# Kernel optimization log

Measured on AMD Instinct MI355X. Metric: run time of the kernel, lower is better.

The kernel has to match this reference:

```python
import jax, jax.numpy as jnp
import numpy as np

D = 512
N_WAY = 64
K_SHOT = 16
N_QUERY = 8192


def setup_inputs() -> dict:
    key = jax.random.key(0)
    k1, k2, k3, k4 = jax.random.split(key, 4)
    support = jax.random.normal(k1, (N_WAY * K_SHOT, D), dtype=jnp.float32)
    query = jax.random.normal(k2, (N_QUERY, D), dtype=jnp.float32)
    # nn.Linear(input_dim, input_dim) params (kaiming-uniform-ish scale)
    bound = 1.0 / np.sqrt(D)
    W = jax.random.uniform(k3, (D, D), minval=-bound, maxval=bound, dtype=jnp.float32)
    b = jax.random.uniform(k4, (D,), minval=-bound, maxval=bound, dtype=jnp.float32)
    return {"support": support, "query": query, "W": W, "b": b,
            "n_way": N_WAY, "k_shot": K_SHOT}


def reference(support, query, W, b, n_way, k_shot):
    # shared linear projection: x @ W^T + b (torch nn.Linear convention)
    support_emb = support @ W.T + b            # [n_way*k_shot, d]
    query_emb = query @ W.T + b                # [n_q, d]
    # class prototypes: mean over the k_shot axis
    prototypes = support_emb.reshape(n_way, k_shot, -1).mean(axis=1)  # [n_way, d]
    # pairwise squared euclidean distances (broadcast sub/square/sum,
    # same math as the torch euclidean_dist)
    diff = query_emb[:, None, :] - prototypes[None, :, :]  # [n_q, n_way, d]
    dists = jnp.sum(diff * diff, axis=-1)                  # [n_q, n_way]
    return dists
```

## Files before the change

kernel.cpp:

```cpp
#include <hip/hip_runtime.h>
#include <hip/hip_bf16.h>

#define D 512
#define NWAY 64
#define KSHOT 16
#define NQ 8192
#define BM 64

typedef __bf16 bf16_t;
typedef __bf16 bf16x8_t __attribute__((ext_vector_type(8)));
typedef __bf16 bf16x4_t __attribute__((ext_vector_type(4)));
typedef float  f32x4    __attribute__((ext_vector_type(4)));

typedef __attribute__((address_space(1))) const void gv_t;
typedef __attribute__((address_space(3))) void lv_t;
__device__ __forceinline__ void ld16(const void* g, void* l) {
    __builtin_amdgcn_global_load_lds((gv_t*)g, (lv_t*)l, 16, 0, 0);
}


__global__ __launch_bounds__(256) void k_prep(
    const float* __restrict__ sup, const float* __restrict__ W,
    const float* __restrict__ bias, bf16_t* __restrict__ Bsw,
    bf16_t* __restrict__ Psw)
{
    const int b = blockIdx.x, t = threadIdx.x;

    if (b < 256) {
        const int c = b >> 2, jq = b & 3;
        __shared__ __align__(16) float cm[D];
        {
            const int d = t * 2;
            float sx = 0.f, sy = 0.f;
#pragma unroll
            for (int j = 0; j < KSHOT; ++j) {
                float2 v = *(const float2*)(sup + (size_t)(c * KSHOT + j) * D + d);
                sx += v.x; sy += v.y;
            }
            cm[d] = sx * (1.0f / KSHOT); cm[d + 1] = sy * (1.0f / KSHOT);
        }
        __syncthreads();
        const int j = jq * 128 + (t >> 1);
        const int half = t & 1;
        const f32x4* wr = (const f32x4*)(W + (size_t)j * D + half * 256);
        const f32x4* cr = (const f32x4*)(cm + half * 256);
        float s = 0.f;
#pragma unroll 8
        for (int i = 0; i < 64; ++i) {
            f32x4 a = cr[i], wv = wr[i];
            s += a[0]*wv[0] + a[1]*wv[1] + a[2]*wv[2] + a[3]*wv[3];
        }
        s += __shfl_xor(s, 1);
        if (!half) {
            const float v = s + bias[j];
            const int sP = j >> 3;
            const int pos = (sP & ~7) | ((sP & 7) ^ (c & 7));
            Psw[c * 512 + pos * 8 + (j & 7)] = (bf16_t)v;
        }
        return;
    }

    {
        const int n = (b - 256) * 4 + (t >> 6);
        const int sl = t & 63;
        const f32x4* wp = (const f32x4*)(W + (size_t)n * D + sl * 8);
        f32x4 v0 = wp[0], v1 = wp[1];
        bf16x8_t hv = { (bf16_t)v0[0], (bf16_t)v0[1], (bf16_t)v0[2], (bf16_t)v0[3],
                        (bf16_t)v1[0], (bf16_t)v1[1], (bf16_t)v1[2], (bf16_t)v1[3] };
        const int ck = sl >> 3, s = sl & 7;
        *(bf16x8_t*)(Bsw + (size_t)ck * 32768 + n * 64 + ((s ^ (n & 7)) * 8)) = hv;
    }
}

__global__ __launch_bounds__(512, 2) void k_main(
    const float* __restrict__ query, const bf16_t* __restrict__ Bsw,
    const bf16_t* __restrict__ Psw, const float* __restrict__ bias,
    float* __restrict__ out)
{
    __shared__ __align__(16) bf16_t Bb[2][32768];
    __shared__ __align__(16) bf16_t Ab[2][4096];
    __shared__ float qln[4][BM];
    __shared__ float phs[NWAY];
    __shared__ float bs[512];

    const int t = threadIdx.x, bm = blockIdx.x;
    bs[t] = bias[t];

    const int l = t & 63, w = t >> 6;
    const int wm = w & 1, wn = w >> 1;
    const int r15 = l & 15, quad = l >> 4;

    const int xt0 = ((quad ^ (r15 & 7)) * 8);
    const int xt1 = (((4 + quad) ^ (r15 & 7)) * 8);
    const int aoff0 = (wm * 32 + r15) * 64;
    const int aoff1 = (wm * 32 + 16 + r15) * 64;
    const int boff = (wn * 128 + r15) * 64;

    const int am = t >> 3;
    const int as = t & 7;
    const int a_lds = am * 64 + ((as ^ (am & 7)) * 8);
    const float* aqp = query + (size_t)(bm * BM + am) * D + as * 8;

    bf16x8_t areg[8];
#pragma unroll
    for (int ck = 0; ck < 8; ++ck) {
        f32x4 v0 = *(const f32x4*)(aqp + ck * 64);
        f32x4 v1 = *(const f32x4*)(aqp + ck * 64 + 4);
        areg[ck] = (bf16x8_t){ (bf16_t)v0[0], (bf16_t)v0[1], (bf16_t)v0[2], (bf16_t)v0[3],
                               (bf16_t)v1[0], (bf16_t)v1[1], (bf16_t)v1[2], (bf16_t)v1[3] };
    }

    f32x4 acc[2][8];
#pragma unroll
    for (int rt = 0; rt < 2; ++rt)
#pragma unroll
        for (int i = 0; i < 8; ++i) acc[rt][i] = (f32x4){0.f, 0.f, 0.f, 0.f};

    {
#pragma unroll
        for (int i = 0; i < 8; ++i) {
            const int off = t * 8 + i * 4096;
            ld16(Bsw + off, &Bb[0][off]);
        }
        *(bf16x8_t*)(&Ab[0][a_lds]) = areg[0];
    }
    __syncthreads();

#pragma unroll
    for (int ck = 0; ck < 8; ++ck) {
        const int cur = ck & 1;
        if (ck < 7) {
            const int nxt = cur ^ 1;
            const size_t sb = (size_t)(ck + 1) * 32768;
#pragma unroll
            for (int i = 0; i < 8; ++i) {
                const int off = t * 8 + i * 4096;
                ld16(Bsw + sb + off, &Bb[nxt][off]);
            }
            *(bf16x8_t*)(&Ab[nxt][a_lds]) = areg[ck + 1];
        } else {
#pragma unroll
            for (int i = 0; i < 8; ++i) {
                const int off = t * 8 + i * 4096;
                ld16(Psw + off, &Bb[0][off]);
            }
        }

        bf16x8_t a00 = *(const bf16x8_t*)(&Ab[cur][aoff0 + xt0]);
        bf16x8_t a01 = *(const bf16x8_t*)(&Ab[cur][aoff0 + xt1]);
        bf16x8_t a10 = *(const bf16x8_t*)(&Ab[cur][aoff1 + xt0]);
        bf16x8_t a11 = *(const bf16x8_t*)(&Ab[cur][aoff1 + xt1]);
#pragma unroll
        for (int tt = 0; tt < 8; ++tt) {
            bf16x8_t b0 = *(const bf16x8_t*)(&Bb[cur][boff + tt * 1024 + xt0]);
            bf16x8_t b1 = *(const bf16x8_t*)(&Bb[cur][boff + tt * 1024 + xt1]);
            acc[0][tt] = __builtin_amdgcn_mfma_f32_16x16x32_bf16(a00, b0, acc[0][tt], 0, 0, 0);
            acc[0][tt] = __builtin_amdgcn_mfma_f32_16x16x32_bf16(a01, b1, acc[0][tt], 0, 0, 0);
            acc[1][tt] = __builtin_amdgcn_mfma_f32_16x16x32_bf16(a10, b0, acc[1][tt], 0, 0, 0);
            acc[1][tt] = __builtin_amdgcn_mfma_f32_16x16x32_bf16(a11, b1, acc[1][tt], 0, 0, 0);
        }

        if (ck < 7) __syncthreads();
    }
    __syncthreads();

    bf16_t* Ex = &Bb[1][0];
    float qp[2][4] = {{0.f,0.f,0.f,0.f},{0.f,0.f,0.f,0.f}};
#pragma unroll
    for (int tt = 0; tt < 8; ++tt) {
        const int k = wn * 128 + tt * 16 + r15;
        const int s = k >> 3, klo = k & 7;
        const float bv = bs[k];
#pragma unroll
        for (int rt = 0; rt < 2; ++rt)
#pragma unroll
        for (int reg = 0; reg < 4; ++reg) {
            const int row = wm * 32 + rt * 16 + quad * 4 + reg;
            const float v = acc[rt][tt][reg] + bv;
            qp[rt][reg] += v * v;
            const int pos = (s & ~7) | ((s & 7) ^ (row & 7));
            Ex[row * 512 + pos * 8 + klo] = (bf16_t)v;
        }
    }
#pragma unroll
    for (int rt = 0; rt < 2; ++rt)
#pragma unroll
    for (int reg = 0; reg < 4; ++reg) {
        float s = qp[rt][reg];
        s += __shfl_xor(s, 1); s += __shfl_xor(s, 2);
        s += __shfl_xor(s, 4); s += __shfl_xor(s, 8);
        if (r15 == 0) qln[wn][wm * 32 + rt * 16 + quad * 4 + reg] = s;
    }

    if (t < NWAY) {
        const bf16_t* pr = &Bb[0][t * 512];
        float s2 = 0.f;
#pragma unroll
        for (int i = 0; i < 64; ++i) {
            bf16x8_t v = *(const bf16x8_t*)(pr + i * 8);
#pragma unroll
            for (int e = 0; e < 8; ++e) { float f = (float)v[e]; s2 += f * f; }
        }
        phs[t] = s2;
    }
    __syncthreads();

    const int ert = w >> 1, ecg = w & 1;
    f32x4 cacc[2];
    cacc[0] = (f32x4){0.f, 0.f, 0.f, 0.f};
    cacc[1] = (f32x4){0.f, 0.f, 0.f, 0.f};
    const bf16_t* Pl = &Bb[0][0];
#pragma unroll
    for (int kk = 0; kk < 16; ++kk) {
        const int s = kk * 4 + quad;
        const int posA = (s & ~7) | ((s & 7) ^ (r15 & 7));
        bf16x8_t af = *(const bf16x8_t*)(Ex + (ert * 16 + r15) * 512 + posA * 8);
#pragma unroll
        for (int j = 0; j < 2; ++j) {
            bf16x8_t bf = *(const bf16x8_t*)(Pl + ((ecg * 2 + j) * 16 + r15) * 512 + posA * 8);
            cacc[j] = __builtin_amdgcn_mfma_f32_16x16x32_bf16(af, bf, cacc[j], 0, 0, 0);
        }
    }

#pragma unroll
    for (int reg = 0; reg < 4; ++reg) {
        const int row_local = ert * 16 + quad * 4 + reg;
        const float qt = qln[0][row_local] + qln[1][row_local] +
                         qln[2][row_local] + qln[3][row_local];
        const int rowg = bm * BM + row_local;
#pragma unroll
        for (int j = 0; j < 2; ++j) {
            const int c = (ecg * 2 + j) * 16 + r15;
            out[(size_t)rowg * NWAY + c] = qt + phs[c] - 2.0f * cacc[j][reg];
        }
    }
}

extern "C" void kernel_launch(void* const* d_in, const int* in_sizes, int n_in,
                              void* d_out, int out_size, void* d_ws, size_t ws_size,
                              hipStream_t stream)
{
    const float* support = (const float*)d_in[0];
    const float* query   = (const float*)d_in[1];
    const float* W       = (const float*)d_in[2];
    const float* bias    = (const float*)d_in[3];
    float* out = (float*)d_out;

    char* ws = (char*)d_ws;
    bf16_t* Bsw = (bf16_t*)ws;
    bf16_t* Psw = (bf16_t*)(ws + 524288);

    k_prep<<<384, 256, 0, stream>>>(support, W, bias, Bsw, Psw);
    k_main<<<128, 512, 0, stream>>>(query, Bsw, Psw, bias, out);
}
```

Baseline: 101.9 us.

## Split projection feature dimension across two blocks with atomic output accumulation

Each query tile is now handled by two blocks, each computing half of the projected features and partial norms and dot products, combined through atomicAdd into a zeroed output. This doubles the grid to fill more CUs and halves LDS per block. It adds a memset, atomic traffic, and duplicated query loading and conversion.

```diff
diff --git a/kernel.cpp b/kernel.cpp
--- a/kernel.cpp
+++ b/kernel.cpp
@@ -5,7 +5,6 @@
 #define NWAY 64
 #define KSHOT 16
 #define NQ 8192
-#define BM 64
 
 typedef __bf16 bf16_t;
 typedef __bf16 bf16x8_t __attribute__((ext_vector_type(8)));
@@ -77,14 +76,17 @@
     const bf16_t* __restrict__ Psw, const float* __restrict__ bias,
     float* __restrict__ out)
 {
-    __shared__ __align__(16) bf16_t Bb[2][32768];
+    __shared__ __align__(16) bf16_t Bb[2][16384];
     __shared__ __align__(16) bf16_t Ab[2][4096];
-    __shared__ float qln[4][BM];
+    __shared__ float qln[4][64];
     __shared__ float phs[NWAY];
-    __shared__ float bs[512];
-
-    const int t = threadIdx.x, bm = blockIdx.x;
-    bs[t] = bias[t];
+    __shared__ float bs[256];
+
+    const int t = threadIdx.x;
+    const int bm = blockIdx.x >> 1;
+    const int h  = blockIdx.x & 1;
+
+    if (t < 256) bs[t] = bias[h * 256 + t];
 
     const int l = t & 63, w = t >> 6;
     const int wm = w & 1, wn = w >> 1;
@@ -94,12 +96,12 @@
     const int xt1 = (((4 + quad) ^ (r15 & 7)) * 8);
     const int aoff0 = (wm * 32 + r15) * 64;
     const int aoff1 = (wm * 32 + 16 + r15) * 64;
-    const int boff = (wn * 128 + r15) * 64;
+    const int boff = (wn * 64 + r15) * 64;
 
     const int am = t >> 3;
     const int as = t & 7;
     const int a_lds = am * 64 + ((as ^ (am & 7)) * 8);
-    const float* aqp = query + (size_t)(bm * BM + am) * D + as * 8;
+    const float* aqp = query + (size_t)(bm * 64 + am) * D + as * 8;
 
     bf16x8_t areg[8];
 #pragma unroll
@@ -110,20 +112,19 @@
                                (bf16_t)v1[0], (bf16_t)v1[1], (bf16_t)v1[2], (bf16_t)v1[3] };
     }
 
-    f32x4 acc[2][8];
+    f32x4 acc[2][4];
 #pragma unroll
     for (int rt = 0; rt < 2; ++rt)
 #pragma unroll
-        for (int i = 0; i < 8; ++i) acc[rt][i] = (f32x4){0.f, 0.f, 0.f, 0.f};
-
-    {
-#pragma unroll
-        for (int i = 0; i < 8; ++i) {
-            const int off = t * 8 + i * 4096;
-            ld16(Bsw + off, &Bb[0][off]);
-        }
-        *(bf16x8_t*)(&Ab[0][a_lds]) = areg[0];
-    }
+        for (int i = 0; i < 4; ++i) acc[rt][i] = (f32x4){0.f, 0.f, 0.f, 0.f};
+
+    const int hbase = h * 16384;
+#pragma unroll
+    for (int i = 0; i < 4; ++i) {
+        const int off = t * 8 + i * 4096;
+        ld16(Bsw + hbase + off, &Bb[0][off]);
+    }
+    *(bf16x8_t*)(&Ab[0][a_lds]) = areg[0];
     __syncthreads();
 
 #pragma unroll
@@ -131,18 +132,19 @@
         const int cur = ck & 1;
         if (ck < 7) {
             const int nxt = cur ^ 1;
-            const size_t sb = (size_t)(ck + 1) * 32768;
-#pragma unroll
-            for (int i = 0; i < 8; ++i) {
+            const size_t sb = (size_t)(ck + 1) * 32768 + hbase;
+#pragma unroll
+            for (int i = 0; i < 4; ++i) {
                 const int off = t * 8 + i * 4096;
                 ld16(Bsw + sb + off, &Bb[nxt][off]);
             }
             *(bf16x8_t*)(&Ab[nxt][a_lds]) = areg[ck + 1];
         } else {
 #pragma unroll
-            for (int i = 0; i < 8; ++i) {
+            for (int i = 0; i < 4; ++i) {
                 const int off = t * 8 + i * 4096;
-                ld16(Psw + off, &Bb[0][off]);
+                const int c = off >> 8, j = off & 255;
+                ld16(Psw + c * 512 + h * 256 + j, &Bb[0][off]);
             }
         }
 
@@ -151,7 +153,7 @@
         bf16x8_t a10 = *(const bf16x8_t*)(&Ab[cur][aoff1 + xt0]);
         bf16x8_t a11 = *(const bf16x8_t*)(&Ab[cur][aoff1 + xt1]);
 #pragma unroll
-        for (int tt = 0; tt < 8; ++tt) {
+        for (int tt = 0; tt < 4; ++tt) {
             bf16x8_t b0 = *(const bf16x8_t*)(&Bb[cur][boff + tt * 1024 + xt0]);
             bf16x8_t b1 = *(const bf16x8_t*)(&Bb[cur][boff + tt * 1024 + xt1]);
             acc[0][tt] = __builtin_amdgcn_mfma_f32_16x16x32_bf16(a00, b0, acc[0][tt], 0, 0, 0);
@@ -167,8 +169,8 @@
     bf16_t* Ex = &Bb[1][0];
     float qp[2][4] = {{0.f,0.f,0.f,0.f},{0.f,0.f,0.f,0.f}};
 #pragma unroll
-    for (int tt = 0; tt < 8; ++tt) {
-        const int k = wn * 128 + tt * 16 + r15;
+    for (int tt = 0; tt < 4; ++tt) {
+        const int k = wn * 64 + tt * 16 + r15;
         const int s = k >> 3, klo = k & 7;
         const float bv = bs[k];
 #pragma unroll
@@ -179,7 +181,7 @@
             const float v = acc[rt][tt][reg] + bv;
             qp[rt][reg] += v * v;
             const int pos = (s & ~7) | ((s & 7) ^ (row & 7));
-            Ex[row * 512 + pos * 8 + klo] = (bf16_t)v;
+            Ex[row * 256 + pos * 8 + klo] = (bf16_t)v;
         }
     }
 #pragma unroll
@@ -193,10 +195,10 @@
     }
 
     if (t < NWAY) {
-        const bf16_t* pr = &Bb[0][t * 512];
+        const bf16_t* pr = &Bb[0][t * 256];
         float s2 = 0.f;
 #pragma unroll
-        for (int i = 0; i < 64; ++i) {
+        for (int i = 0; i < 32; ++i) {
             bf16x8_t v = *(const bf16x8_t*)(pr + i * 8);
 #pragma unroll
             for (int e = 0; e < 8; ++e) { float f = (float)v[e]; s2 += f * f; }
@@ -205,33 +207,34 @@
     }
     __syncthreads();
 
-    const int ert = w >> 1, ecg = w & 1;
+    const int rt2 = w >> 1, cg = w & 1;
     f32x4 cacc[2];
     cacc[0] = (f32x4){0.f, 0.f, 0.f, 0.f};
     cacc[1] = (f32x4){0.f, 0.f, 0.f, 0.f};
     const bf16_t* Pl = &Bb[0][0];
 #pragma unroll
-    for (int kk = 0; kk < 16; ++kk) {
+    for (int kk = 0; kk < 8; ++kk) {
         const int s = kk * 4 + quad;
         const int posA = (s & ~7) | ((s & 7) ^ (r15 & 7));
-        bf16x8_t af = *(const bf16x8_t*)(Ex + (ert * 16 + r15) * 512 + posA * 8);
+        bf16x8_t af = *(const bf16x8_t*)(Ex + (rt2 * 16 + r15) * 256 + posA * 8);
 #pragma unroll
         for (int j = 0; j < 2; ++j) {
-            bf16x8_t bf = *(const bf16x8_t*)(Pl + ((ecg * 2 + j) * 16 + r15) * 512 + posA * 8);
+            bf16x8_t bf = *(const bf16x8_t*)(Pl + ((cg * 2 + j) * 16 + r15) * 256 + posA * 8);
             cacc[j] = __builtin_amdgcn_mfma_f32_16x16x32_bf16(af, bf, cacc[j], 0, 0, 0);
         }
     }
 
 #pragma unroll
     for (int reg = 0; reg < 4; ++reg) {
-        const int row_local = ert * 16 + quad * 4 + reg;
+        const int row_local = rt2 * 16 + quad * 4 + reg;
         const float qt = qln[0][row_local] + qln[1][row_local] +
                          qln[2][row_local] + qln[3][row_local];
-        const int rowg = bm * BM + row_local;
+        const int rowg = bm * 64 + row_local;
 #pragma unroll
         for (int j = 0; j < 2; ++j) {
-            const int c = (ecg * 2 + j) * 16 + r15;
-            out[(size_t)rowg * NWAY + c] = qt + phs[c] - 2.0f * cacc[j][reg];
+            const int c = (cg * 2 + j) * 16 + r15;
+            atomicAdd(&out[(size_t)rowg * NWAY + c],
+                      qt + phs[c] - 2.0f * cacc[j][reg]);
         }
     }
 }
@@ -250,6 +253,7 @@
     bf16_t* Bsw = (bf16_t*)ws;
     bf16_t* Psw = (bf16_t*)(ws + 524288);
 
+    hipMemsetAsync(out, 0, (size_t)NQ * NWAY * sizeof(float), stream);
     k_prep<<<384, 256, 0, stream>>>(support, W, bias, Bsw, Psw);
-    k_main<<<128, 512, 0, stream>>>(query, Bsw, Psw, bias, out);
-}
+    k_main<<<256, 512, 0, stream>>>(query, Bsw, Psw, bias, out);
+}
```

Result: no change. 102.3 us (+0.4%).
